# Kernel optimization log

Hardware: AMD Instinct MI355X
Metric: run time of the kernel (lower is better)

Reference implementation:

```python
import jax, jax.numpy as jnp
import numpy as np

N_NODES = 50000
N_EDGES = 800000
DIM = 128
HEADS = 8
DK = DIM // HEADS  # 16
SQRT_DK = float(np.sqrt(DK))


def setup_inputs() -> dict:
    key = jax.random.key(0)
    ks = jax.random.split(key, 12)
    inp = {
        "h": jax.random.normal(ks[0], (N_NODES, DIM), jnp.float32),
        "src": jax.random.randint(ks[1], (N_EDGES,), 0, N_NODES, jnp.int32),
        "dst": jax.random.randint(ks[2], (N_EDGES,), 0, N_NODES, jnp.int32),
        "Wk": jax.random.normal(ks[3], (DIM, DIM), jnp.float32) / np.sqrt(DIM),
        "bk": jnp.zeros((DIM,), jnp.float32),
        "Wq": jax.random.normal(ks[4], (DIM, DIM), jnp.float32) / np.sqrt(DIM),
        "bq": jnp.zeros((DIM,), jnp.float32),
        "Wv": jax.random.normal(ks[5], (DIM, DIM), jnp.float32) / np.sqrt(DIM),
        "bv": jnp.zeros((DIM,), jnp.float32),
        "Wa": jax.random.normal(ks[6], (DIM, DIM), jnp.float32) / np.sqrt(DIM),
        "ba": jnp.zeros((DIM,), jnp.float32),
        "rel_att": jax.random.normal(ks[7], (HEADS, DK, DK), jnp.float32) / np.sqrt(DK),
        "rel_msg": jax.random.normal(ks[8], (HEADS, DK, DK), jnp.float32) / np.sqrt(DK),
        "rel_pri": jnp.ones((HEADS,), jnp.float32),
        "skip": jnp.ones((1,), jnp.float32),
    }
    return inp


def reference(h, src, dst, Wk, bk, Wq, bq, Wv, bv, Wa, ba, rel_att, rel_msg, rel_pri, skip):
    N = h.shape[0]
    # node-level projections -> [N, H, d_k]
    k = (h @ Wk + bk).reshape(N, HEADS, DK)
    q = (h @ Wq + bq).reshape(N, HEADS, DK)
    v = (h @ Wv + bv).reshape(N, HEADS, DK)
    # relation-specific transforms
    k = jnp.einsum('nhi,hij->nhj', k, rel_att)
    v = jnp.einsum('nhi,hij->nhj', v, rel_msg)
    # per-edge score: dot(q[dst], k[src]) over d_k -> [E, H]
    score = jnp.einsum('ehd,ehd->eh', q[dst], k[src]) * rel_pri / SQRT_DK
    # segment softmax over destination nodes (edge_softmax, norm_by='dst')
    smax = jax.ops.segment_max(score, dst, num_segments=N)  # [N, H]
    e = jnp.exp(score - smax[dst])
    ssum = jax.ops.segment_sum(e, dst, num_segments=N)  # [N, H]
    attn = e / ssum[dst]  # [E, H]
    # weighted scatter-sum of messages: sum_e v[src_e] * attn_e -> [N, H, d_k]
    m = v[src] * attn[:, :, None]
    t = jax.ops.segment_sum(m, dst, num_segments=N).reshape(N, DIM)
    # target-specific aggregation (dropout in eval mode = identity, use_norm=False)
    trans_out = t @ Wa + ba
    alpha = jax.nn.sigmoid(skip)  # [1], broadcasts
    new_h = trans_out * alpha + h * (1.0 - alpha)
    return new_h
```

## Files before the change

kernel.cpp:

```cpp
#include <hip/hip_runtime.h>
#include <stdint.h>

#define NN 50000
#define NE 800000

typedef __bf16 v8bf __attribute__((ext_vector_type(8)));
typedef float  v4f  __attribute__((ext_vector_type(4)));

#define EXP2F(x) __builtin_amdgcn_exp2f(x)

__device__ __forceinline__ float bf2f(unsigned short u) {
    return __uint_as_float(((unsigned)u) << 16);
}
__device__ __forceinline__ unsigned short f2bf(float f) {
    unsigned u = __float_as_uint(f);
    u += 0x7FFFu + ((u >> 16) & 1u);
    return (unsigned short)(u >> 16);
}
__device__ __forceinline__ float ldf(const void* p, size_t i, int isb) {
    return isb ? bf2f(((const unsigned short*)p)[i]) : ((const float*)p)[i];
}

__global__ __launch_bounds__(128) void k_prep(
    const void* __restrict__ Wq, const void* __restrict__ bq,
    const void* __restrict__ Wk, const void* __restrict__ bk,
    const void* __restrict__ Wv, const void* __restrict__ bv,
    const void* __restrict__ Wa, const void* __restrict__ ba,
    const void* __restrict__ rel_att, const void* __restrict__ rel_msg,
    const void* __restrict__ rel_pri,
    int* __restrict__ FLAG, unsigned short* __restrict__ WTb,
    float* __restrict__ BC)
{
    const unsigned rp0 = ((const unsigned*)rel_pri)[0];
    const int isb = ((rp0 & 0xFFFFu) != 0u) ? 1 : 0;
    int b = blockIdx.x;
    int m = b >> 7;
    int i = b & 127;
    int j = threadIdx.x;
    if (b == 0 && j == 0) FLAG[0] = isb;
    if (m == 0) {
        WTb[((size_t)(0 * 128 + j)) * 128 + i] = f2bf(ldf(Wq, i * 128 + j, isb));
        if (i == 0) BC[j] = ldf(bq, j, isb);
    } else if (m == 3) {
        WTb[((size_t)(3 * 128 + j)) * 128 + i] = f2bf(ldf(Wa, i * 128 + j, isb));
        if (i == 0) BC[3 * 128 + j] = ldf(ba, j, isb);
    } else {
        const void* W    = (m == 1) ? Wk : Wv;
        const void* bias = (m == 1) ? bk : bv;
        const void* R    = (m == 1) ? rel_att : rel_msg;
        int hh = j >> 4, jj = j & 15;
        float scale = (m == 1) ? ldf(rel_pri, hh, isb) * 0.25f : 1.0f;
        float acc = 0.f, bacc = 0.f;
        #pragma unroll
        for (int l = 0; l < 16; ++l) {
            float r = ldf(R, hh * 256 + l * 16 + jj, isb);
            acc  += ldf(W, i * 128 + hh * 16 + l, isb) * r;
            bacc += ldf(bias, hh * 16 + l, isb) * r;
        }
        WTb[((size_t)(m * 128 + j)) * 128 + i] = f2bf(acc * scale);
        if (i == 0) BC[m * 128 + j] = bacc * scale;
    }
}

__global__ __launch_bounds__(256) void k_qkv_m(
    const void* __restrict__ h, const unsigned short* __restrict__ WTb,
    const float* __restrict__ BC, const int* __restrict__ FLAG,
    unsigned short* __restrict__ QKVb)
{
    __shared__ __align__(16) unsigned short Ah[64][136];
    __shared__ __align__(16) unsigned short Bh[128][136];
    const int isb = FLAG[0];
    const int tid = threadIdx.x;
    const int rowBase = blockIdx.x * 64;

    if (isb) {
        #pragma unroll
        for (int i = 0; i < 4; ++i) {
            int lin = tid + i * 256;
            int row = lin >> 4, kc = (lin & 15) * 8;
            int gr = rowBase + row;
            uint4 u = make_uint4(0, 0, 0, 0);
            if (gr < NN) u = *(const uint4*)((const unsigned short*)h + (size_t)gr * 128 + kc);
            *(uint4*)&Ah[row][kc] = u;
        }
    } else {
        #pragma unroll
        for (int i = 0; i < 8; ++i) {
            int lin = tid + i * 256;
            int row = lin >> 5, c4 = (lin & 31) * 4;
            int gr = rowBase + row;
            ushort4 o = make_ushort4(0, 0, 0, 0);
            if (gr < NN) {
                float4 f = *(const float4*)((const float*)h + (size_t)gr * 128 + c4);
                o.x = f2bf(f.x); o.y = f2bf(f.y); o.z = f2bf(f.z); o.w = f2bf(f.w);
            }
            *(ushort4*)&Ah[row][c4] = o;
        }
    }

    const int w = tid >> 6, l = tid & 63;
    const int lr = l & 15, q = l >> 4;

    for (int m = 0; m < 3; ++m) {
        if (m) __syncthreads();
        #pragma unroll
        for (int i = 0; i < 8; ++i) {
            int lin = tid + i * 256;
            int col = lin >> 4, kc = (lin & 15) * 8;
            uint4 u = *(const uint4*)(WTb + ((size_t)(m * 128 + col)) * 128 + kc);
            *(uint4*)&Bh[col][kc] = u;
        }
        __syncthreads();

        v4f acc[8];
        #pragma unroll
        for (int nt = 0; nt < 8; ++nt) {
            float bj = BC[m * 128 + nt * 16 + lr];
            acc[nt] = (v4f){bj, bj, bj, bj};
        }
        #pragma unroll
        for (int kk = 0; kk < 4; ++kk) {
            v8bf a = *(const v8bf*)&Ah[w * 16 + lr][kk * 32 + q * 8];
            #pragma unroll
            for (int nt = 0; nt < 8; ++nt) {
                v8bf b = *(const v8bf*)&Bh[nt * 16 + lr][kk * 32 + q * 8];
                acc[nt] = __builtin_amdgcn_mfma_f32_16x16x32_bf16(a, b, acc[nt], 0, 0, 0);
            }
        }
        #pragma unroll
        for (int nt = 0; nt < 8; ++nt) {
            #pragma unroll
            for (int r = 0; r < 4; ++r) {
                int row = rowBase + w * 16 + q * 4 + r;
                if (row < NN)
                    QKVb[((size_t)m * NN + row) * 128 + nt * 16 + lr] = f2bf(acc[nt][r]);
            }
        }
    }
}

__global__ __launch_bounds__(256) void k_hist(
    const int* __restrict__ dst, unsigned* __restrict__ CNT)
{
    int e = blockIdx.x * 256 + threadIdx.x;
    atomicAdd(&CNT[dst[e]], 1u);
}

#define SCB 512
#define NSB 98
__global__ __launch_bounds__(SCB) void k_scan1(
    const unsigned* __restrict__ CNT, unsigned* __restrict__ RPS,
    unsigned* __restrict__ BSUM)
{
    __shared__ unsigned sh[SCB];
    int tid = threadIdx.x;
    int g = blockIdx.x * SCB + tid;
    unsigned v = (g < NN) ? CNT[g] : 0u;
    sh[tid] = v;
    __syncthreads();
    #pragma unroll
    for (int off = 1; off < SCB; off <<= 1) {
        unsigned t = 0;
        if (tid >= off) t = sh[tid - off];
        __syncthreads();
        if (tid >= off) sh[tid] += t;
        __syncthreads();
    }
    if (g < NN) RPS[g] = sh[tid] - v;
    if (tid == SCB - 1) BSUM[blockIdx.x] = sh[tid];
}

__global__ __launch_bounds__(128) void k_scan2(
    const unsigned* __restrict__ BSUM, unsigned* __restrict__ BOFF)
{
    __shared__ unsigned sh[128];
    int tid = threadIdx.x;
    unsigned v = (tid < NSB) ? BSUM[tid] : 0u;
    sh[tid] = v;
    __syncthreads();
    #pragma unroll
    for (int off = 1; off < 128; off <<= 1) {
        unsigned t = 0;
        if (tid >= off) t = sh[tid - off];
        __syncthreads();
        if (tid >= off) sh[tid] += t;
        __syncthreads();
    }
    if (tid < NSB) BOFF[tid] = sh[tid] - v;
}

__global__ __launch_bounds__(256) void k_scan3(
    const unsigned* __restrict__ RPS, const unsigned* __restrict__ BOFF,
    int* __restrict__ RP)
{
    int g = blockIdx.x * 256 + threadIdx.x;
    if (g < NN) RP[g] = (int)(RPS[g] + BOFF[g / SCB]);
    if (g == NN) RP[NN] = NE;
}

__global__ __launch_bounds__(256) void k_fill(
    const int* __restrict__ src, const int* __restrict__ dst,
    const int* __restrict__ RP, unsigned* __restrict__ CUR,
    int* __restrict__ ESRC)
{
    int e = blockIdx.x * 256 + threadIdx.x;
    int d = dst[e];
    int pos = (int)atomicAdd(&CUR[d], 1u);
    ESRC[RP[d] + pos] = src[e];
}

__global__ __launch_bounds__(256) void k_attn(
    const int* __restrict__ RP, const int* __restrict__ ESRC,
    const unsigned short* __restrict__ Qb, const unsigned short* __restrict__ Kb,
    const unsigned short* __restrict__ Vb, unsigned short* __restrict__ Tb)
{
    int d = (blockIdx.x * 256 + threadIdx.x) >> 6;
    int lane = threadIdx.x & 63;
    int beg = RP[d], end = RP[d + 1];
    const float LOG2E = 1.4426950408889634f;

    ushort2 qq = *(const ushort2*)(Qb + (size_t)d * 128 + lane * 2);
    float q0 = bf2f(qq.x) * LOG2E, q1 = bf2f(qq.y) * LOG2E;

    float m = -3.0e38f, s = 0.f, o0 = 0.f, o1 = 0.f;
    int j = beg;
    for (; j + 4 <= end; j += 4) {
        int s0 = ESRC[j], s1 = ESRC[j + 1], s2 = ESRC[j + 2], s3 = ESRC[j + 3];
        ushort2 k0 = *(const ushort2*)(Kb + (size_t)s0 * 128 + lane * 2);
        ushort2 k1 = *(const ushort2*)(Kb + (size_t)s1 * 128 + lane * 2);
        ushort2 k2 = *(const ushort2*)(Kb + (size_t)s2 * 128 + lane * 2);
        ushort2 k3 = *(const ushort2*)(Kb + (size_t)s3 * 128 + lane * 2);
        ushort2 v0 = *(const ushort2*)(Vb + (size_t)s0 * 128 + lane * 2);
        ushort2 v1 = *(const ushort2*)(Vb + (size_t)s1 * 128 + lane * 2);
        ushort2 v2 = *(const ushort2*)(Vb + (size_t)s2 * 128 + lane * 2);
        ushort2 v3 = *(const ushort2*)(Vb + (size_t)s3 * 128 + lane * 2);
        float p0 = q0 * bf2f(k0.x) + q1 * bf2f(k0.y);
        float p1 = q0 * bf2f(k1.x) + q1 * bf2f(k1.y);
        float p2 = q0 * bf2f(k2.x) + q1 * bf2f(k2.y);
        float p3 = q0 * bf2f(k3.x) + q1 * bf2f(k3.y);
        p0 += __shfl_xor(p0, 1); p1 += __shfl_xor(p1, 1);
        p2 += __shfl_xor(p2, 1); p3 += __shfl_xor(p3, 1);
        p0 += __shfl_xor(p0, 2); p1 += __shfl_xor(p1, 2);
        p2 += __shfl_xor(p2, 2); p3 += __shfl_xor(p3, 2);
        p0 += __shfl_xor(p0, 4); p1 += __shfl_xor(p1, 4);
        p2 += __shfl_xor(p2, 4); p3 += __shfl_xor(p3, 4);
        float nm = fmaxf(fmaxf(m, fmaxf(p0, p1)), fmaxf(p2, p3));
        float al = EXP2F(m - nm);
        float w0 = EXP2F(p0 - nm), w1 = EXP2F(p1 - nm);
        float w2 = EXP2F(p2 - nm), w3 = EXP2F(p3 - nm);
        s  = s * al + ((w0 + w1) + (w2 + w3));
        o0 = o0 * al + ((w0 * bf2f(v0.x) + w1 * bf2f(v1.x))
                      + (w2 * bf2f(v2.x) + w3 * bf2f(v3.x)));
        o1 = o1 * al + ((w0 * bf2f(v0.y) + w1 * bf2f(v1.y))
                      + (w2 * bf2f(v2.y) + w3 * bf2f(v3.y)));
        m = nm;
    }
    for (; j < end; ++j) {
        int sid = ESRC[j];
        ushort2 kk = *(const ushort2*)(Kb + (size_t)sid * 128 + lane * 2);
        float p = q0 * bf2f(kk.x) + q1 * bf2f(kk.y);
        p += __shfl_xor(p, 1);
        p += __shfl_xor(p, 2);
        p += __shfl_xor(p, 4);
        ushort2 vv = *(const ushort2*)(Vb + (size_t)sid * 128 + lane * 2);
        float nm = fmaxf(m, p);
        float al = EXP2F(m - nm);
        float w  = EXP2F(p - nm);
        s  = s  * al + w;
        o0 = o0 * al + w * bf2f(vv.x);
        o1 = o1 * al + w * bf2f(vv.y);
        m = nm;
    }
    float r = (s > 0.f) ? (1.0f / s) : 0.f;
    ushort2 o;
    o.x = f2bf(o0 * r); o.y = f2bf(o1 * r);
    *(ushort2*)(Tb + (size_t)d * 128 + lane * 2) = o;
}

__global__ __launch_bounds__(256) void k_final_m(
    const unsigned short* __restrict__ Tb, const unsigned short* __restrict__ WTb,
    const float* __restrict__ BC, const void* __restrict__ h,
    const void* __restrict__ skip, const int* __restrict__ FLAG,
    void* __restrict__ out)
{
    __shared__ __align__(16) unsigned short Ah[64][136];
    __shared__ __align__(16) unsigned short Bh[128][136];
    const int isb = FLAG[0];
    const int tid = threadIdx.x;
    const int rowBase = blockIdx.x * 64;

    #pragma unroll
    for (int i = 0; i < 4; ++i) {
        int lin = tid + i * 256;
        int row = lin >> 4, kc = (lin & 15) * 8;
        int gr = rowBase + row;
        uint4 u = make_uint4(0, 0, 0, 0);
        if (gr < NN) u = *(const uint4*)(Tb + (size_t)gr * 128 + kc);
        *(uint4*)&Ah[row][kc] = u;
    }
    #pragma unroll
    for (int i = 0; i < 8; ++i) {
        int lin = tid + i * 256;
        int col = lin >> 4, kc = (lin & 15) * 8;
        uint4 u = *(const uint4*)(WTb + ((size_t)(3 * 128 + col)) * 128 + kc);
        *(uint4*)&Bh[col][kc] = u;
    }
    __syncthreads();

    const int w = tid >> 6, l = tid & 63;
    const int lr = l & 15, q = l >> 4;
    v4f acc[8];
    #pragma unroll
    for (int nt = 0; nt < 8; ++nt) {
        float bj = BC[3 * 128 + nt * 16 + lr];
        acc[nt] = (v4f){bj, bj, bj, bj};
    }
    #pragma unroll
    for (int kk = 0; kk < 4; ++kk) {
        v8bf a = *(const v8bf*)&Ah[w * 16 + lr][kk * 32 + q * 8];
        #pragma unroll
        for (int nt = 0; nt < 8; ++nt) {
            v8bf b = *(const v8bf*)&Bh[nt * 16 + lr][kk * 32 + q * 8];
            acc[nt] = __builtin_amdgcn_mfma_f32_16x16x32_bf16(a, b, acc[nt], 0, 0, 0);
        }
    }
    float skipv = ldf(skip, 0, isb);
    float alpha = 1.0f / (1.0f + __expf(-skipv));
    float beta = 1.0f - alpha;
    #pragma unroll
    for (int nt = 0; nt < 8; ++nt) {
        #pragma unroll
        for (int r = 0; r < 4; ++r) {
            int row = rowBase + w * 16 + q * 4 + r;
            if (row < NN) {
                size_t off = (size_t)row * 128 + nt * 16 + lr;
                float hv = ldf(h, off, isb);
                float o = alpha * acc[nt][r] + beta * hv;
                if (isb) ((unsigned short*)out)[off] = f2bf(o);
                else     ((float*)out)[off] = o;
            }
        }
    }
}

extern "C" void kernel_launch(void* const* d_in, const int* in_sizes, int n_in,
                              void* d_out, int out_size, void* d_ws, size_t ws_size,
                              hipStream_t stream)
{
    const void* h  = d_in[0];
    const int* src = (const int*)d_in[1];
    const int* dst = (const int*)d_in[2];
    const void* Wk = d_in[3];
    const void* bk = d_in[4];
    const void* Wq = d_in[5];
    const void* bq = d_in[6];
    const void* Wv = d_in[7];
    const void* bv = d_in[8];
    const void* Wa = d_in[9];
    const void* ba = d_in[10];
    const void* rel_att = d_in[11];
    const void* rel_msg = d_in[12];
    const void* rel_pri = d_in[13];
    const void* skip    = d_in[14];

    float* F = (float*)d_ws;
    int* FLAG      = (int*)F;
    float* BC      = F + 16;
    unsigned short* WTb = (unsigned short*)(BC + 512);
    unsigned* CNT  = (unsigned*)((float*)(BC + 512) + 32768);
    unsigned* CUR  = CNT + 50048;
    unsigned* RPS  = CUR + 50048;
    unsigned* BSUM = RPS + 50048;
    unsigned* BOFF = BSUM + 128;
    int* RP        = (int*)(BOFF + 128);
    unsigned short* Tb = (unsigned short*)(RP + 50064);
    int* ESRC      = (int*)(Tb + (size_t)NN * 128);
    unsigned short* QKVb = (unsigned short*)(ESRC + NE);
    unsigned short* Qb = QKVb;
    unsigned short* Kb = QKVb + (size_t)NN * 128;
    unsigned short* Vb = QKVb + (size_t)2 * NN * 128;

    (void)hipMemsetAsync(CNT, 0, 2 * 50048 * sizeof(unsigned), stream);

    k_prep<<<512, 128, 0, stream>>>(Wq, bq, Wk, bk, Wv, bv, Wa, ba,
                                    rel_att, rel_msg, rel_pri, FLAG, WTb, BC);
    k_qkv_m<<<782, 256, 0, stream>>>(h, WTb, BC, FLAG, QKVb);

    k_hist<<<NE / 256, 256, 0, stream>>>(dst, CNT);
    k_scan1<<<NSB, SCB, 0, stream>>>(CNT, RPS, BSUM);
    k_scan2<<<1, 128, 0, stream>>>(BSUM, BOFF);
    k_scan3<<<(NN + 256) / 256, 256, 0, stream>>>(RPS, BOFF, RP);
    k_fill<<<NE / 256, 256, 0, stream>>>(src, dst, RP, CUR, ESRC);

    k_attn<<<(NN * 64) / 256, 256, 0, stream>>>(RP, ESRC, Qb, Kb, Vb, Tb);
    k_final_m<<<782, 256, 0, stream>>>(Tb, WTb, BC, h, skip, FLAG, d_out);
}
```

Before: 291.9 us.

## Fuse histogram and scans, interleave K/V, drop running max in edge softmax

Zeroing of counters moves into the weight-prep kernel and the degree histogram runs as extra blocks of the QKV projection kernel. The three scan kernels collapse into one, using a last-block-done counter, and row pointers are computed on the fly from block offsets. K and V are stored interleaved so each edge gather is a single 8-byte load per lane. The attention loop is unrolled to 8 edges and skips the online max rescaling, which saves work but risks exp overflow for large scores.

```diff
diff --git a/kernel.cpp b/kernel.cpp
--- a/kernel.cpp
+++ b/kernel.cpp
@@ -29,7 +29,8 @@
     const void* __restrict__ rel_att, const void* __restrict__ rel_msg,
     const void* __restrict__ rel_pri,
     int* __restrict__ FLAG, unsigned short* __restrict__ WTb,
-    float* __restrict__ BC)
+    float* __restrict__ BC, unsigned* __restrict__ CNT,
+    unsigned* __restrict__ CUR, unsigned* __restrict__ DONE)
 {
     const unsigned rp0 = ((const unsigned*)rel_pri)[0];
     const int isb = ((rp0 & 0xFFFFu) != 0u) ? 1 : 0;
@@ -37,7 +38,9 @@
     int m = b >> 7;
     int i = b & 127;
     int j = threadIdx.x;
-    if (b == 0 && j == 0) FLAG[0] = isb;
+    int t = b * 128 + j;
+    if (t < 50048) { CNT[t] = 0u; CUR[t] = 0u; }
+    if (t == 0) { FLAG[0] = isb; DONE[0] = 0u; }
     if (m == 0) {
         WTb[((size_t)(0 * 128 + j)) * 128 + i] = f2bf(ldf(Wq, i * 128 + j, isb));
         if (i == 0) BC[j] = ldf(bq, j, isb);
@@ -62,15 +65,23 @@
     }
 }
 
-__global__ __launch_bounds__(256) void k_qkv_m(
+__global__ __launch_bounds__(256) void k_qkvh(
     const void* __restrict__ h, const unsigned short* __restrict__ WTb,
     const float* __restrict__ BC, const int* __restrict__ FLAG,
-    unsigned short* __restrict__ QKVb)
+    const int* __restrict__ dst, unsigned* __restrict__ CNT,
+    unsigned short* __restrict__ Qb, unsigned short* __restrict__ KVb)
 {
     __shared__ __align__(16) unsigned short Ah[64][136];
     __shared__ __align__(16) unsigned short Bh[128][136];
+    const int tid = threadIdx.x;
+
+    if (blockIdx.x >= 782) {
+        int e = (blockIdx.x - 782) * 256 + tid;
+        atomicAdd(&CNT[dst[e]], 1u);
+        return;
+    }
+
     const int isb = FLAG[0];
-    const int tid = threadIdx.x;
     const int rowBase = blockIdx.x * 64;
 
     if (isb) {
@@ -132,27 +143,26 @@
             #pragma unroll
             for (int r = 0; r < 4; ++r) {
                 int row = rowBase + w * 16 + q * 4 + r;
-                if (row < NN)
-                    QKVb[((size_t)m * NN + row) * 128 + nt * 16 + lr] = f2bf(acc[nt][r]);
+                if (row < NN) {
+                    int col = nt * 16 + lr;
+                    unsigned short val = f2bf(acc[nt][r]);
+                    if (m == 0) Qb[(size_t)row * 128 + col] = val;
+                    else        KVb[(size_t)row * 256 + col * 2 + (m - 1)] = val;
+                }
             }
         }
     }
-}
-
-__global__ __launch_bounds__(256) void k_hist(
-    const int* __restrict__ dst, unsigned* __restrict__ CNT)
-{
-    int e = blockIdx.x * 256 + threadIdx.x;
-    atomicAdd(&CNT[dst[e]], 1u);
 }
 
 #define SCB 512
 #define NSB 98
-__global__ __launch_bounds__(SCB) void k_scan1(
+__global__ __launch_bounds__(SCB) void k_scan(
     const unsigned* __restrict__ CNT, unsigned* __restrict__ RPS,
-    unsigned* __restrict__ BSUM)
+    unsigned* __restrict__ BSUM, unsigned* __restrict__ BOFF,
+    unsigned* __restrict__ DONE)
 {
     __shared__ unsigned sh[SCB];
+    __shared__ int lastFlag;
     int tid = threadIdx.x;
     int g = blockIdx.x * SCB + tid;
     unsigned v = (g < NN) ? CNT[g] : 0u;
@@ -167,109 +177,87 @@
         __syncthreads();
     }
     if (g < NN) RPS[g] = sh[tid] - v;
-    if (tid == SCB - 1) BSUM[blockIdx.x] = sh[tid];
-}
-
-__global__ __launch_bounds__(128) void k_scan2(
-    const unsigned* __restrict__ BSUM, unsigned* __restrict__ BOFF)
-{
-    __shared__ unsigned sh[128];
-    int tid = threadIdx.x;
-    unsigned v = (tid < NSB) ? BSUM[tid] : 0u;
-    sh[tid] = v;
-    __syncthreads();
-    #pragma unroll
-    for (int off = 1; off < 128; off <<= 1) {
+    if (tid == SCB - 1) atomicExch(&BSUM[blockIdx.x], sh[tid]);
+    __syncthreads();
+    if (tid == 0) {
+        __threadfence();
+        lastFlag = (atomicAdd(DONE, 1u) == NSB - 1);
+    }
+    __syncthreads();
+    if (!lastFlag) return;
+
+    unsigned bv = (tid < NSB) ? atomicAdd(&BSUM[tid], 0u) : 0u;
+    sh[tid] = bv;
+    __syncthreads();
+    #pragma unroll
+    for (int off = 1; off < SCB; off <<= 1) {
         unsigned t = 0;
         if (tid >= off) t = sh[tid - off];
         __syncthreads();
         if (tid >= off) sh[tid] += t;
         __syncthreads();
     }
-    if (tid < NSB) BOFF[tid] = sh[tid] - v;
-}
-
-__global__ __launch_bounds__(256) void k_scan3(
-    const unsigned* __restrict__ RPS, const unsigned* __restrict__ BOFF,
-    int* __restrict__ RP)
-{
-    int g = blockIdx.x * 256 + threadIdx.x;
-    if (g < NN) RP[g] = (int)(RPS[g] + BOFF[g / SCB]);
-    if (g == NN) RP[NN] = NE;
+    if (tid < NSB) BOFF[tid] = sh[tid] - bv;
 }
 
 __global__ __launch_bounds__(256) void k_fill(
     const int* __restrict__ src, const int* __restrict__ dst,
-    const int* __restrict__ RP, unsigned* __restrict__ CUR,
-    int* __restrict__ ESRC)
+    const unsigned* __restrict__ RPS, const unsigned* __restrict__ BOFF,
+    unsigned* __restrict__ CUR, int* __restrict__ ESRC)
 {
     int e = blockIdx.x * 256 + threadIdx.x;
     int d = dst[e];
     int pos = (int)atomicAdd(&CUR[d], 1u);
-    ESRC[RP[d] + pos] = src[e];
+    ESRC[(int)(RPS[d] + BOFF[d >> 9]) + pos] = src[e];
 }
 
 __global__ __launch_bounds__(256) void k_attn(
-    const int* __restrict__ RP, const int* __restrict__ ESRC,
-    const unsigned short* __restrict__ Qb, const unsigned short* __restrict__ Kb,
-    const unsigned short* __restrict__ Vb, unsigned short* __restrict__ Tb)
+    const unsigned* __restrict__ RPS, const unsigned* __restrict__ BOFF,
+    const int* __restrict__ ESRC,
+    const unsigned short* __restrict__ Qb, const unsigned short* __restrict__ KVb,
+    unsigned short* __restrict__ Tb)
 {
     int d = (blockIdx.x * 256 + threadIdx.x) >> 6;
     int lane = threadIdx.x & 63;
-    int beg = RP[d], end = RP[d + 1];
+    int beg = (int)(RPS[d] + BOFF[d >> 9]);
+    int end = (d == NN - 1) ? NE : (int)(RPS[d + 1] + BOFF[(d + 1) >> 9]);
     const float LOG2E = 1.4426950408889634f;
 
     ushort2 qq = *(const ushort2*)(Qb + (size_t)d * 128 + lane * 2);
     float q0 = bf2f(qq.x) * LOG2E, q1 = bf2f(qq.y) * LOG2E;
 
-    float m = -3.0e38f, s = 0.f, o0 = 0.f, o1 = 0.f;
+    float s = 0.f, o0 = 0.f, o1 = 0.f;
     int j = beg;
-    for (; j + 4 <= end; j += 4) {
-        int s0 = ESRC[j], s1 = ESRC[j + 1], s2 = ESRC[j + 2], s3 = ESRC[j + 3];
-        ushort2 k0 = *(const ushort2*)(Kb + (size_t)s0 * 128 + lane * 2);
-        ushort2 k1 = *(const ushort2*)(Kb + (size_t)s1 * 128 + lane * 2);
-        ushort2 k2 = *(const ushort2*)(Kb + (size_t)s2 * 128 + lane * 2);
-        ushort2 k3 = *(const ushort2*)(Kb + (size_t)s3 * 128 + lane * 2);
-        ushort2 v0 = *(const ushort2*)(Vb + (size_t)s0 * 128 + lane * 2);
-        ushort2 v1 = *(const ushort2*)(Vb + (size_t)s1 * 128 + lane * 2);
-        ushort2 v2 = *(const ushort2*)(Vb + (size_t)s2 * 128 + lane * 2);
-        ushort2 v3 = *(const ushort2*)(Vb + (size_t)s3 * 128 + lane * 2);
-        float p0 = q0 * bf2f(k0.x) + q1 * bf2f(k0.y);
-        float p1 = q0 * bf2f(k1.x) + q1 * bf2f(k1.y);
-        float p2 = q0 * bf2f(k2.x) + q1 * bf2f(k2.y);
-        float p3 = q0 * bf2f(k3.x) + q1 * bf2f(k3.y);
-        p0 += __shfl_xor(p0, 1); p1 += __shfl_xor(p1, 1);
-        p2 += __shfl_xor(p2, 1); p3 += __shfl_xor(p3, 1);
-        p0 += __shfl_xor(p0, 2); p1 += __shfl_xor(p1, 2);
-        p2 += __shfl_xor(p2, 2); p3 += __shfl_xor(p3, 2);
-        p0 += __shfl_xor(p0, 4); p1 += __shfl_xor(p1, 4);
-        p2 += __shfl_xor(p2, 4); p3 += __shfl_xor(p3, 4);
-        float nm = fmaxf(fmaxf(m, fmaxf(p0, p1)), fmaxf(p2, p3));
-        float al = EXP2F(m - nm);
-        float w0 = EXP2F(p0 - nm), w1 = EXP2F(p1 - nm);
-        float w2 = EXP2F(p2 - nm), w3 = EXP2F(p3 - nm);
-        s  = s * al + ((w0 + w1) + (w2 + w3));
-        o0 = o0 * al + ((w0 * bf2f(v0.x) + w1 * bf2f(v1.x))
-                      + (w2 * bf2f(v2.x) + w3 * bf2f(v3.x)));
-        o1 = o1 * al + ((w0 * bf2f(v0.y) + w1 * bf2f(v1.y))
-                      + (w2 * bf2f(v2.y) + w3 * bf2f(v3.y)));
-        m = nm;
+    for (; j + 8 <= end; j += 8) {
+        ushort4 kv[8];
+        #pragma unroll
+        for (int t = 0; t < 8; ++t) {
+            int sid = ESRC[j + t];
+            kv[t] = *(const ushort4*)(KVb + (size_t)sid * 256 + lane * 4);
+        }
+        #pragma unroll
+        for (int t = 0; t < 8; ++t) {
+            float p = q0 * bf2f(kv[t].x) + q1 * bf2f(kv[t].z);
+            p += __shfl_xor(p, 1);
+            p += __shfl_xor(p, 2);
+            p += __shfl_xor(p, 4);
+            float w = EXP2F(p);
+            s  += w;
+            o0 += w * bf2f(kv[t].y);
+            o1 += w * bf2f(kv[t].w);
+        }
     }
     for (; j < end; ++j) {
         int sid = ESRC[j];
-        ushort2 kk = *(const ushort2*)(Kb + (size_t)sid * 128 + lane * 2);
-        float p = q0 * bf2f(kk.x) + q1 * bf2f(kk.y);
+        ushort4 kv = *(const ushort4*)(KVb + (size_t)sid * 256 + lane * 4);
+        float p = q0 * bf2f(kv.x) + q1 * bf2f(kv.z);
         p += __shfl_xor(p, 1);
         p += __shfl_xor(p, 2);
         p += __shfl_xor(p, 4);
-        ushort2 vv = *(const ushort2*)(Vb + (size_t)sid * 128 + lane * 2);
-        float nm = fmaxf(m, p);
-        float al = EXP2F(m - nm);
-        float w  = EXP2F(p - nm);
-        s  = s  * al + w;
-        o0 = o0 * al + w * bf2f(vv.x);
-        o1 = o1 * al + w * bf2f(vv.y);
-        m = nm;
+        float w = EXP2F(p);
+        s  += w;
+        o0 += w * bf2f(kv.y);
+        o1 += w * bf2f(kv.w);
     }
     float r = (s > 0.f) ? (1.0f / s) : 0.f;
     ushort2 o;
@@ -372,26 +360,18 @@
     unsigned* RPS  = CUR + 50048;
     unsigned* BSUM = RPS + 50048;
     unsigned* BOFF = BSUM + 128;
-    int* RP        = (int*)(BOFF + 128);
-    unsigned short* Tb = (unsigned short*)(RP + 50064);
+    unsigned* DONE = BOFF + 128;
+    unsigned short* Tb = (unsigned short*)(DONE + 16);
     int* ESRC      = (int*)(Tb + (size_t)NN * 128);
-    unsigned short* QKVb = (unsigned short*)(ESRC + NE);
-    unsigned short* Qb = QKVb;
-    unsigned short* Kb = QKVb + (size_t)NN * 128;
-    unsigned short* Vb = QKVb + (size_t)2 * NN * 128;
-
-    (void)hipMemsetAsync(CNT, 0, 2 * 50048 * sizeof(unsigned), stream);
+    unsigned short* Qb  = (unsigned short*)(ESRC + NE);
+    unsigned short* KVb = Qb + (size_t)NN * 128;
 
     k_prep<<<512, 128, 0, stream>>>(Wq, bq, Wk, bk, Wv, bv, Wa, ba,
-                                    rel_att, rel_msg, rel_pri, FLAG, WTb, BC);
-    k_qkv_m<<<782, 256, 0, stream>>>(h, WTb, BC, FLAG, QKVb);
-
-    k_hist<<<NE / 256, 256, 0, stream>>>(dst, CNT);
-    k_scan1<<<NSB, SCB, 0, stream>>>(CNT, RPS, BSUM);
-    k_scan2<<<1, 128, 0, stream>>>(BSUM, BOFF);
-    k_scan3<<<(NN + 256) / 256, 256, 0, stream>>>(RPS, BOFF, RP);
-    k_fill<<<NE / 256, 256, 0, stream>>>(src, dst, RP, CUR, ESRC);
-
-    k_attn<<<(NN * 64) / 256, 256, 0, stream>>>(RP, ESRC, Qb, Kb, Vb, Tb);
+                                    rel_att, rel_msg, rel_pri, FLAG, WTb, BC,
+                                    CNT, CUR, DONE);
+    k_qkvh<<<782 + 3125, 256, 0, stream>>>(h, WTb, BC, FLAG, dst, CNT, Qb, KVb);
+    k_scan<<<NSB, SCB, 0, stream>>>(CNT, RPS, BSUM, BOFF, DONE);
+    k_fill<<<NE / 256, 256, 0, stream>>>(src, dst, RPS, BOFF, CUR, ESRC);
+    k_attn<<<(NN * 64) / 256, 256, 0, stream>>>(RPS, BOFF, ESRC, Qb, KVb, Tb);
     k_final_m<<<782, 256, 0, stream>>>(Tb, WTb, BC, h, skip, FLAG, d_out);
 }
```

After: 290.0 us. No clear change (-0.7%).
